# Kernel tuning notes

Measured on AMD Instinct MI355X. Metric: run time of the kernel, lower is better.

## Reference

```python
import jax, jax.numpy as jnp
import numpy as np

B, T, DNA_DIM = 8, 8192, 4
HID, C, K = 256, 5, 16
NEG = -1e30


def setup_inputs() -> dict:
    key = jax.random.key(0)
    ks = jax.random.split(key, 9)
    sequence = jax.random.normal(ks[0], (B, T, DNA_DIM), dtype=jnp.float32)
    lengths = jax.random.randint(ks[1], (B,), T // 2, T + 1).astype(jnp.int32)
    W_enc = jax.random.normal(ks[2], (DNA_DIM, HID), dtype=jnp.float32) * 0.1
    b_enc = jnp.zeros((HID,), dtype=jnp.float32)
    W_proj = jax.random.normal(ks[3], (HID, C), dtype=jnp.float32) * 0.05
    b_proj = jnp.zeros((C,), dtype=jnp.float32)
    trans = jax.random.normal(ks[4], (C, C), dtype=jnp.float32) * 0.1
    start = jax.random.normal(ks[5], (C,), dtype=jnp.float32) * 0.1
    dur = jax.random.normal(ks[6], (C, K), dtype=jnp.float32) * 0.1  # learned duration scores
    return {"sequence": sequence, "lengths": lengths, "W_enc": W_enc, "b_enc": b_enc,
            "W_proj": W_proj, "b_proj": b_proj, "trans": trans, "start": start, "dur": dur}


def reference(sequence, lengths, W_enc, b_enc, W_proj, b_proj, trans, start, dur):
    """Encoder + semi-Markov CRF head forward.

    Returns (partition, cum_scores):
      partition  : (B,) log partition function over all segmentations up to `lengths`.
      cum_scores : (B, T+1, C) cumulative per-class emission scores (segment score
                   for span (s, t] with label c is cum[t, c] - cum[s, c]).
    """
    # --- encoder: pointwise linear + GELU ---
    hidden = jax.nn.gelu(sequence @ W_enc + b_enc)          # (B, T, HID)
    emit = hidden @ W_proj + b_proj                          # (B, T, C)

    # --- cumulative segment scores ---
    cum = jnp.concatenate(
        [jnp.zeros((B, 1, C), emit.dtype), jnp.cumsum(emit, axis=1)], axis=1
    )                                                        # (B, T+1, C)

    # prevs[:, t-1, d-1, :] = cum[:, t-d, :]   (zero-padded for t-d < 0; masked by H)
    cum_pad = jnp.pad(cum, ((0, 0), (K, 0), (0, 0)))         # (B, T+1+K, C)
    prevs = jnp.stack(
        [cum_pad[:, K - d + 1: K - d + 1 + T, :] for d in range(1, K + 1)], axis=2
    )                                                        # (B, T, K, C)
    cur = cum[:, 1:, :]                                      # (B, T, C)

    dur_t = dur.T                                            # (K, C)

    # --- semi-Markov forward DP via scan; carry = last K transition-folded alphas ---
    # H[:, d-1, :] = m[t-d] where m[j, c] = logsumexp_{c'} alpha[j, c'] + trans[c', c]
    # and m[0] = start scores.
    H0 = jnp.full((B, K, C), NEG, dtype=emit.dtype).at[:, 0, :].set(start[None, :])

    def step(H, xs):
        cur_t, prev_t = xs                                   # (B, C), (B, K, C)
        seg = cur_t[:, None, :] - prev_t                     # segment emission scores
        score = H + seg + dur_t[None, :, :]                  # (B, K, C)
        alpha = jax.nn.logsumexp(score, axis=1)              # (B, C)
        m = jax.nn.logsumexp(alpha[:, :, None] + trans[None, :, :], axis=1)  # (B, C)
        Hn = jnp.concatenate([m[:, None, :], H[:, :-1, :]], axis=1)
        return Hn, alpha

    xs = (jnp.swapaxes(cur, 0, 1), jnp.swapaxes(prevs, 0, 1))
    _, alphas = jax.lax.scan(step, H0, xs)                   # (T, B, C)

    alpha_L = alphas[lengths - 1, jnp.arange(B)]             # (B, C) at each sequence end
    partition = jax.nn.logsumexp(alpha_L, axis=-1)           # (B,)
    return partition, cum
```

## Files before the change

### kernel.cpp

```cpp
#include <hip/hip_runtime.h>
#include <hip/hip_bf16.h>

#define B_ 8
#define T_ 8192
#define HID_ 256
#define C_ 5
#define K_ 16
#define NC_ 32
#define NTILE 32
#define GSPAN 272
#define GW 276
#define GIOFF (5 * GW)
#define NFW 15

__device__ __forceinline__ float gelu_tanh(float x) {
    float u = 0.7978845608028654f * (x + 0.044715f * x * x * x);
    float e = __expf(2.0f * u);
    float th = 1.0f - 2.0f / (e + 1.0f);
    return 0.5f * x * (1.0f + th);
}

__device__ __forceinline__ float bf16lo(unsigned int u) {
    return __uint_as_float(u << 16);
}
__device__ __forceinline__ float bf16hi(unsigned int u) {
    return __uint_as_float(u & 0xffff0000u);
}
template <int CTRL>
__device__ __forceinline__ float dppf(float x) {
    return __uint_as_float((unsigned int)__builtin_amdgcn_mov_dpp(
        (int)__float_as_uint(x), CTRL, 0xF, 0xF, true));
}

__global__ __launch_bounds__(256) void encoder_kernel(
    const float* __restrict__ seq, const float* __restrict__ W_enc,
    const float* __restrict__ b_enc, const float* __restrict__ W_proj,
    const float* __restrict__ b_proj, float* __restrict__ emitA,
    float* __restrict__ emitB, float* __restrict__ PA)
{
    __shared__ float4 we[128];
    __shared__ float  be[128];
    __shared__ float  wp[128 * C_];
    __shared__ float  prd[4][C_];
    int tid = threadIdx.x;
    int half = blockIdx.x >> 8;
    int blk  = blockIdx.x & 255;
    int h0 = half * 128;
    if (tid < 128) {
        int h = h0 + tid;
        we[tid] = make_float4(W_enc[0*HID_+h], W_enc[1*HID_+h], W_enc[2*HID_+h], W_enc[3*HID_+h]);
        be[tid] = b_enc[h];
    }
    for (int i = tid; i < 128 * C_; i += 256) wp[i] = W_proj[h0 * C_ + i];
    __syncthreads();
    int b = blk >> 5;
    int tile = blk & 31;
    int t = tile * 256 + tid;
    float4 s = reinterpret_cast<const float4*>(seq)[(size_t)b * T_ + t];
    float a0, a1, a2, a3, a4;
    if (half == 0) { a0 = b_proj[0]; a1 = b_proj[1]; a2 = b_proj[2]; a3 = b_proj[3]; a4 = b_proj[4]; }
    else           { a0 = a1 = a2 = a3 = a4 = 0.0f; }
    #pragma unroll 8
    for (int h = 0; h < 128; ++h) {
        float4 w = we[h];
        float pre = be[h] + s.x*w.x + s.y*w.y + s.z*w.z + s.w*w.w;
        float hd = gelu_tanh(pre);
        a0 = fmaf(hd, wp[h*C_+0], a0);
        a1 = fmaf(hd, wp[h*C_+1], a1);
        a2 = fmaf(hd, wp[h*C_+2], a2);
        a3 = fmaf(hd, wp[h*C_+3], a3);
        a4 = fmaf(hd, wp[h*C_+4], a4);
    }
    float* em = half ? emitB : emitA;
    size_t base = (size_t)b * C_ * T_ + t;
    em[base + 0*T_] = a0;
    em[base + 1*T_] = a1;
    em[base + 2*T_] = a2;
    em[base + 3*T_] = a3;
    em[base + 4*T_] = a4;
    float s0 = a0, s1 = a1, s2 = a2, s3 = a3, s4 = a4;
    #pragma unroll
    for (int off = 1; off < 64; off <<= 1) {
        s0 += __shfl_xor(s0, off, 64);
        s1 += __shfl_xor(s1, off, 64);
        s2 += __shfl_xor(s2, off, 64);
        s3 += __shfl_xor(s3, off, 64);
        s4 += __shfl_xor(s4, off, 64);
    }
    int lane = tid & 63, wv = tid >> 6;
    if (lane == 0) { prd[wv][0]=s0; prd[wv][1]=s1; prd[wv][2]=s2; prd[wv][3]=s3; prd[wv][4]=s4; }
    __syncthreads();
    if (tid < C_) {
        float t4 = (prd[0][tid] + prd[1][tid]) + (prd[2][tid] + prd[3][tid]);
        PA[((half * B_ + b) * NTILE + tile) * C_ + tid] = t4;
    }
}

__global__ __launch_bounds__(64) void cumwrite_kernel(
    const float* __restrict__ emitA, const float* __restrict__ emitB,
    const float* __restrict__ PA, float* __restrict__ cum)
{
    int bx = blockIdx.x;
    int tile = bx & (NTILE - 1);
    int bc = bx >> 5;
    int b = bc / C_, c = bc - b * C_;
    int lane = threadIdx.x;
    float v = 0.0f;
    if (lane < NTILE && lane < tile)
        v = PA[((0 * B_ + b) * NTILE + lane) * C_ + c]
          + PA[((1 * B_ + b) * NTILE + lane) * C_ + c];
    #pragma unroll
    for (int o = 32; o; o >>= 1) v += __shfl_xor(v, o, 64);
    const float* eA = emitA + ((size_t)b * C_ + c) * T_;
    const float* eB = emitB + ((size_t)b * C_ + c) * T_;
    float* cb = cum + (size_t)b * (T_ + 1) * C_;
    if (tile == 0 && lane == 0) cb[c] = 0.0f;
    float carry = v;
    #pragma unroll
    for (int i = 0; i < 4; ++i) {
        int idx = tile * 256 + i * 64 + lane;
        float e = eA[idx] + eB[idx];
        float si = e;
        #pragma unroll
        for (int o = 1; o < 64; o <<= 1) {
            float n = __shfl_up(si, o, 64);
            if (lane >= o) si += n;
        }
        cb[(size_t)(idx + 1) * C_ + c] = carry + si;
        carry += __shfl(si, 63, 64);
    }
}

#define DOT16(PP, OUT)                                                        \
    {                                                                         \
        float q0, q1, q2, q3;                                                 \
        q0 = W[0] * ed[(0 + (PP)) & 15];                                      \
        q1 = W[1] * ed[(1 + (PP)) & 15];                                      \
        q2 = W[2] * ed[(2 + (PP)) & 15];                                      \
        q3 = W[3] * ed[(3 + (PP)) & 15];                                      \
        q0 = fmaf(W[4],  ed[(4  + (PP)) & 15], q0);                           \
        q1 = fmaf(W[5],  ed[(5  + (PP)) & 15], q1);                           \
        q2 = fmaf(W[6],  ed[(6  + (PP)) & 15], q2);                           \
        q3 = fmaf(W[7],  ed[(7  + (PP)) & 15], q3);                           \
        q0 = fmaf(W[8],  ed[(8  + (PP)) & 15], q0);                           \
        q1 = fmaf(W[9],  ed[(9  + (PP)) & 15], q1);                           \
        q2 = fmaf(W[10], ed[(10 + (PP)) & 15], q2);                           \
        q3 = fmaf(W[11], ed[(11 + (PP)) & 15], q3);                           \
        q0 = fmaf(W[12], ed[(12 + (PP)) & 15], q0);                           \
        q1 = fmaf(W[13], ed[(13 + (PP)) & 15], q1);                           \
        q2 = fmaf(W[14], ed[(14 + (PP)) & 15], q2);                           \
        q3 = fmaf(W[15], ed[(15 + (PP)) & 15], q3);                           \
        OUT = (q0 + q1) + (q2 + q3);                                          \
    }

#define CSTEP(PP, GV, GIV, CAP)                                               \
    {                                                                         \
        P *= (GV); iP *= (GIV);                                               \
        float dtv;                                                            \
        DOT16(PP, dtv);                                                       \
        acur = P * dtv;                                                       \
        float r3  = dppf<0x113>(acur);                         \
        float r6  = dppf<0x116>(acur);                         \
        float r9  = dppf<0x119>(acur);                         \
        float r12 = dppf<0x11C>(acur);                         \
        float l3  = dppf<0x103>(acur);                         \
        float l6  = dppf<0x106>(acur);                         \
        float l9  = dppf<0x109>(acur);                         \
        float l12 = dppf<0x10C>(acur);                         \
        if (CAP) {                                                            \
            A0v = fmaf(a0w0, acur, fmaf(a0w1, r3, fmaf(a0w2, r6,              \
                  fmaf(a0w3, r9, a0w4 * r12))));                              \
        }                                                                     \
        float Sn = fmaf(wSelf, acur,                                          \
                   fmaf(wL1, r3,  fmaf(wL2, r6,  fmaf(wL3, r9,                \
                   fmaf(wL4, r12, fmaf(wR1, l3,  fmaf(wR2, l6,                \
                   fmaf(wR3, l9,  wR4 * l12))))))));                          \
        W[15 - (PP)] = Sn * iP;                                               \
    }

#define CRENORM()                                                             \
    {                                                                         \
        bool ok = (A0v > 1e-30f);                                             \
        float rr = ok ? __builtin_amdgcn_rcpf(A0v) : 1.0f;                    \
        float lz = ok ? __logf(A0v) : 0.0f;                                   \
        float f = P * rr;                                                     \
        _Pragma("unroll") for (int q = 0; q < 16; ++q) W[q] *= f;             \
        P = 1.0f; iP = 1.0f; z += lz;                                         \
    }

#define QBLK(Q)                                                               \
    {                                                                         \
        float4 vg  = *reinterpret_cast<const float4*>(gpg + tl0 + (Q));       \
        float4 vgi = *reinterpret_cast<const float4*>(gpi + tl0 + (Q));       \
        CSTEP((Q)+0, vg.x, vgi.x, 0); CSTEP((Q)+1, vg.y, vgi.y, 0);           \
        CSTEP((Q)+2, vg.z, vgi.z, 0);                                         \
        CSTEP((Q)+3, vg.w, vgi.w, ((Q) == 4 || (Q) == 12));                   \
    }

#define TS(PP, GV, GIV)                                                       \
    if ((PP) < rem) {                                                         \
        CSTEP(PP, GV, GIV, ((PP) == 7 || (PP) == 15));                        \
        if ((PP) == rem - 1) Afin = acur;                                     \
        if ((((PP) & 7) == 7) && ((PP) < rem - 1)) CRENORM();                 \
    }

#define TQ(Q)                                                                 \
    if ((Q) < rem) {                                                          \
        float4 vg  = *reinterpret_cast<const float4*>(gpg + tl0 + (Q));       \
        float4 vgi = *reinterpret_cast<const float4*>(gpi + tl0 + (Q));       \
        TS((Q)+0, vg.x, vgi.x); TS((Q)+1, vg.y, vgi.y);                       \
        TS((Q)+2, vg.z, vgi.z); TS((Q)+3, vg.w, vgi.w);                       \
    }

__global__ __launch_bounds__(448) void chunk_kernel(
    const float* __restrict__ emitA, const float* __restrict__ emitB,
    const int* __restrict__ lengths, const float* __restrict__ trans,
    const float* __restrict__ dur, __hip_bfloat16* __restrict__ Mout,
    float* __restrict__ Rout, float* __restrict__ ezOut,
    float* __restrict__ Zmx)
{
    __shared__ float gg[2 * 5 * GW];
    __shared__ float zsh[80];
    __shared__ float zred;
    int blk = blockIdx.x;
    int b = blk >> 5, k = blk & (NC_ - 1);
    int len = lengths[b];
    int s = (k * len) >> 5;
    int e = ((k + 1) * len) >> 5;
    int L = e - s;
    int tid = threadIdx.x;

    for (int i = tid; i < C_ * GSPAN; i += 448) {
        int cc = i / GSPAN, j = i - cc * GSPAN;
        int pos = s - 16 + j;
        float g = 1.0f, gi = 1.0f;
        if (pos >= 0 && j < 16 + L) {
            size_t gx = ((size_t)b * C_ + cc) * T_ + pos;
            float ev = emitA[gx] + emitB[gx];
            g = __expf(ev); gi = __expf(-ev);
        }
        gg[cc * GW + j] = g;
        gg[GIOFF + cc * GW + j] = gi;
    }
    __syncthreads();

    int lane = tid & 63, wv = tid >> 6;
    int row16 = lane >> 4;
    int sub = lane & 15;
    int c = sub / 3; if (c > 4) c = 4;
    int colIdx = sub - c * 3;
    int col = wv * 12 + row16 * 3 + colIdx;
    bool active = (sub < 15) && (col < 80);

    const float* gpg = &gg[c * GW + 16];
    const float* gpi = &gg[GIOFF + c * GW + 16];

    float ed[K_];
    #pragma unroll
    for (int j = 0; j < K_; ++j) ed[j] = __expf(dur[c * K_ + j]);

    float gate = active ? 1.0f : 0.0f;
    float eTf[C_];
    #pragma unroll
    for (int x = 0; x < C_; ++x) eTf[x] = __expf(trans[x * C_ + c]) * gate;
    float wSelf = eTf[c];
    float wL1 = (c >= 1) ? eTf[c-1] : 0.0f;
    float wL2 = (c >= 2) ? eTf[c-2] : 0.0f;
    float wL3 = (c >= 3) ? eTf[c-3] : 0.0f;
    float wL4 = (c >= 4) ? eTf[c-4] : 0.0f;
    float wR1 = (c + 1 <= 4) ? eTf[c+1] : 0.0f;
    float wR2 = (c + 2 <= 4) ? eTf[c+2] : 0.0f;
    float wR3 = (c + 3 <= 4) ? eTf[c+3] : 0.0f;
    float wR4 = (c + 4 <= 4) ? eTf[c+4] : 0.0f;
    float a0w0 = (c == 0) ? gate : 0.0f;
    float a0w1 = (c == 1) ? gate : 0.0f;
    float a0w2 = (c == 2) ? gate : 0.0f;
    float a0w3 = (c == 3) ? gate : 0.0f;
    float a0w4 = (c == 4) ? gate : 0.0f;

    int j0 = col / 5, c0 = col - j0 * 5;
    float sv = 1.0f;
    for (int j = 16 - j0; j < 16; ++j) sv *= gg[c0 * GW + j];
    float W[K_];
    #pragma unroll
    for (int q = 0; q < K_; ++q)
        W[q] = (active && c == c0 && q == j0) ? sv : 0.0f;

    float P = 1.0f, iP = 1.0f, z = 0.0f;
    float acur = 0.0f, Afin = 0.0f, A0v = 0.0f;

    int nfull = (L - 1) >> 4;
    int rem = L - (nfull << 4);
    int tl0 = 0;

    for (int bi = 0; bi < nfull; ++bi) {
        QBLK(0); QBLK(4);
        CRENORM();
        QBLK(8); QBLK(12);
        CRENORM();
        tl0 += 16;
    }
    TQ(0); TQ(4); TQ(8); TQ(12);

    size_t cid = (size_t)b * NC_ + k;
    int pn = L & 15;
    if (k == NC_ - 1) {
        if (active) {
            Rout[(size_t)b * 400 + (size_t)col * C_ + c] = Afin;
            if (c == 0) zsh[col] = z;
        }
    } else {
        float lm = 0.0f;
        if (active) {
            #pragma unroll
            for (int slot = 0; slot < K_; ++slot) {
                int j = (slot + pn) & 15;
                float pr = 1.0f;
                for (int i2 = 0; i2 < j; ++i2)
                    pr *= gg[GIOFF + c * GW + 16 + L - 1 - i2];
                float vv = W[slot] * P * pr;
                W[slot] = vv;
                lm = fmaxf(lm, vv);
            }
        }
        float m = lm;
        m = fmaxf(m, dppf<0x103>(lm)); m = fmaxf(m, dppf<0x106>(lm));
        m = fmaxf(m, dppf<0x109>(lm)); m = fmaxf(m, dppf<0x10C>(lm));
        m = fmaxf(m, dppf<0x113>(lm)); m = fmaxf(m, dppf<0x116>(lm));
        m = fmaxf(m, dppf<0x119>(lm)); m = fmaxf(m, dppf<0x11C>(lm));
        float cmax = m;
        float inv = (cmax > 0.0f) ? 1.0f / cmax : 0.0f;
        if (active) {
            __hip_bfloat16* mb = Mout + cid * 6400 + (size_t)col * 80;
            #pragma unroll
            for (int slot = 0; slot < K_; ++slot) {
                int j = (slot + pn) & 15;
                mb[j * C_ + c] = __float2bfloat16(W[slot] * inv);
            }
            if (c == 0) zsh[col] = (cmax > 0.0f) ? z + __logf(cmax) : -3.0e38f;
        }
    }
    __syncthreads();
    if (tid < 64) {
        float m = zsh[tid];
        if (tid < 16) m = fmaxf(m, zsh[tid + 64]);
        #pragma unroll
        for (int off = 32; off; off >>= 1) m = fmaxf(m, __shfl_xor(m, off, 64));
        if (tid == 0) zred = m;
    }
    __syncthreads();
    float zm = zred;
    if (tid == 0) Zmx[cid] = zm;
    if (active && c == 0) ezOut[cid * 80 + col] = __expf(zsh[col] - zm);
}

__global__ __launch_bounds__(320) void chain_kernel(
    const __hip_bfloat16* __restrict__ Mst, const float* __restrict__ ezZ,
    const float* __restrict__ Zmx, const float* __restrict__ Rst,
    const float* __restrict__ startv, float* __restrict__ Uvec,
    float* __restrict__ Xvec, float* __restrict__ Zu, float* __restrict__ Zx)
{
    __shared__ float Ml[2][80 * 82];
    __shared__ float vin[80], sv[80], part[4][80];
    __shared__ float red;
    int b = blockIdx.x >> 1;
    int dir = blockIdx.x & 1;
    int tid = threadIdx.x;
    float Z = 0.0f;
    int nmat = (dir == 0) ? NFW : (NC_ - 1 - NFW);

    if (dir == 0) {
        if (tid < 80) vin[tid] = (tid < C_) ? __expf(startv[tid]) : 0.0f;
        __syncthreads();
    } else {
        size_t last = (size_t)b * NC_ + NC_ - 1;
        if (tid < 80) {
            const float* R = Rst + (size_t)b * 400 + (size_t)tid * C_;
            float rs = ((R[0] + R[1]) + (R[2] + R[3])) + R[4];
            sv[tid] = rs * ezZ[last * 80 + tid];
        }
        __syncthreads();
        if (tid < 64) {
            float m = sv[tid];
            if (tid < 16) m = fmaxf(m, sv[tid + 64]);
            #pragma unroll
            for (int o = 32; o; o >>= 1) m = fmaxf(m, __shfl_xor(m, o, 64));
            if (tid == 0) red = m;
        }
        __syncthreads();
        float rm = red;
        if (tid < 80) vin[tid] = sv[tid] / rm;
        Z = Zmx[b * NC_ + NC_ - 1] + __logf(rm);
        __syncthreads();
    }

    int mk0 = (dir == 0) ? 0 : NC_ - 2;
    {
        const unsigned int* mg = (const unsigned int*)(Mst + (size_t)(b * NC_ + mk0) * 6400);
        #pragma unroll
        for (int i = 0; i < 10; ++i) {
            unsigned int u = mg[tid + 320 * i];
            int idx = (tid + 320 * i) * 2;
            int r = idx / 80, cc = idx - r * 80;
            Ml[0][r * 82 + cc]     = bf16lo(u);
            Ml[0][r * 82 + cc + 1] = bf16hi(u);
        }
    }
    __syncthreads();

    int cur = 0;
    int grp = tid / 80, r = tid - grp * 80;
    for (int it = 0; it < nmat; ++it) {
        int k  = (dir == 0) ? it : (NC_ - 2 - it);
        int kn = (dir == 0) ? k + 1 : k - 1;
        bool more = (it + 1 < nmat);
        size_t cid = (size_t)b * NC_ + k;

        unsigned int mu[10];
        if (more) {
            const unsigned int* mg = (const unsigned int*)(Mst + ((size_t)b * NC_ + kn) * 6400);
            #pragma unroll
            for (int i = 0; i < 10; ++i) mu[i] = mg[tid + 320 * i];
        }
        float ezv = 0.0f;
        if (tid < 80) {
            ezv = ezZ[cid * 80 + tid];
            sv[tid] = (dir == 0) ? vin[tid] * ezv : vin[tid];
        }
        __syncthreads();

        float p = 0.0f;
        if (dir == 0) {
            int q0 = grp * 20;
            #pragma unroll
            for (int i = 0; i < 20; ++i)
                p = fmaf(Ml[cur][(q0 + i) * 82 + r], sv[q0 + i], p);
        } else {
            int rowb = grp * 20;
            #pragma unroll
            for (int i = 0; i < 20; ++i)
                p = fmaf(Ml[cur][r * 82 + rowb + i], sv[rowb + i], p);
        }
        part[grp][r] = p;
        if (more) {
            #pragma unroll
            for (int i = 0; i < 10; ++i) {
                unsigned int u = mu[i];
                int idx = (tid + 320 * i) * 2;
                int rr = idx / 80, cc = idx - rr * 80;
                Ml[cur ^ 1][rr * 82 + cc]     = bf16lo(u);
                Ml[cur ^ 1][rr * 82 + cc + 1] = bf16hi(u);
            }
        }
        __syncthreads();

        Z += Zmx[cid];
        bool rn = ((it & 3) == 3) || (it == nmat - 1);
        if (tid < 80) {
            float nv = (part[0][tid] + part[1][tid]) + (part[2][tid] + part[3][tid]);
            if (dir == 1) nv *= ezv;
            if (rn) sv[tid] = nv; else vin[tid] = nv;
        }
        if (rn) {
            __syncthreads();
            if (tid < 64) {
                float m = sv[tid];
                if (tid < 16) m = fmaxf(m, sv[tid + 64]);
                #pragma unroll
                for (int o = 32; o; o >>= 1) m = fmaxf(m, __shfl_xor(m, o, 64));
                if (tid == 0) red = m;
            }
            __syncthreads();
            float rm = red;
            if (tid < 80) vin[tid] = sv[tid] / rm;
            Z += __logf(rm);
        }
        cur ^= 1;
    }

    if (dir == 0) {
        if (tid < 80) Xvec[b * 80 + tid] = vin[tid];
        if (tid == 0) Zx[b] = Z;
    } else {
        if (tid < 80) Uvec[b * 80 + tid] = vin[tid];
        if (tid == 0) Zu[b] = Z;
    }
}

__global__ __launch_bounds__(512) void meet_kernel(
    const float* __restrict__ Uvec, const float* __restrict__ Xvec,
    const float* __restrict__ Zu, const float* __restrict__ Zx,
    float* __restrict__ partition)
{
    int tid = threadIdx.x;
    int b = tid >> 6, lane = tid & 63;
    float v = Uvec[b * 80 + lane] * Xvec[b * 80 + lane];
    if (lane < 16) v += Uvec[b * 80 + 64 + lane] * Xvec[b * 80 + 64 + lane];
    #pragma unroll
    for (int off = 32; off; off >>= 1) v += __shfl_xor(v, off, 64);
    if (lane == 0) partition[b] = Zu[b] + Zx[b] + __logf(v);
}

extern "C" void kernel_launch(void* const* d_in, const int* in_sizes, int n_in,
                              void* d_out, int out_size, void* d_ws, size_t ws_size,
                              hipStream_t stream) {
    (void)in_sizes; (void)n_in; (void)out_size; (void)ws_size;
    const float* seq    = (const float*)d_in[0];
    const int*   lens   = (const int*)  d_in[1];
    const float* W_enc  = (const float*)d_in[2];
    const float* b_enc  = (const float*)d_in[3];
    const float* W_proj = (const float*)d_in[4];
    const float* b_proj = (const float*)d_in[5];
    const float* trans  = (const float*)d_in[6];
    const float* startv = (const float*)d_in[7];
    const float* dur    = (const float*)d_in[8];

    float* out       = (float*)d_out;
    float* partition = out;
    float* cum       = out + B_;

    float* emitA = (float*)d_ws;
    float* emitB = emitA + (size_t)B_ * C_ * T_;
    __hip_bfloat16* Mst = (__hip_bfloat16*)(emitB + (size_t)B_ * C_ * T_);
    float* Rst = (float*)(Mst + (size_t)B_ * NC_ * 6400);
    float* ezS = Rst + (size_t)B_ * 400;
    float* Zmx = ezS + (size_t)B_ * NC_ * 80;
    float* PA  = Zmx + (size_t)B_ * NC_;
    float* Uv  = PA  + 2 * B_ * NTILE * C_;
    float* Xv  = Uv  + B_ * 80;
    float* Zu  = Xv  + B_ * 80;
    float* Zx  = Zu  + B_;

    encoder_kernel<<<512, 256, 0, stream>>>(seq, W_enc, b_enc, W_proj, b_proj, emitA, emitB, PA);
    chunk_kernel<<<B_ * NC_, 448, 0, stream>>>(emitA, emitB, lens, trans, dur, Mst, Rst, ezS, Zmx);
    cumwrite_kernel<<<B_ * C_ * NTILE, 64, 0, stream>>>(emitA, emitB, PA, cum);
    chain_kernel<<<16, 320, 0, stream>>>(Mst, ezS, Zmx, Rst, startv, Uv, Xv, Zu, Zx);
    meet_kernel<<<1, 512, 0, stream>>>(Uv, Xv, Zu, Zx, partition);
}
```

Baseline: 92.45 us.

## Store chain matrices in per-thread layout and drop LDS staging in chain kernel

The producer now writes the 80x80 bf16 transfer matrices transposed for forward-direction chunks, so each chain thread owns a contiguous run of 20 elements it can load straight into registers. The chain kernel no longer unpacks matrices into a double-buffered shared array. It keeps the current matrix in registers, prefetches the next one, and reads the input vector with float4 loads. Renormalisation now runs every 8 steps instead of every 4, which cuts barriers and reductions but leaves more room for values to grow between rescales. Per-thread global loads of 10 consecutive words are less coalesced than the previous strided pattern.

After: 87.61 us. 1.06x faster.

```diff
diff --git a/kernel.cpp b/kernel.cpp
--- a/kernel.cpp
+++ b/kernel.cpp
@@ -331,11 +331,19 @@
         float cmax = m;
         float inv = (cmax > 0.0f) ? 1.0f / cmax : 0.0f;
         if (active) {
-            __hip_bfloat16* mb = Mout + cid * 6400 + (size_t)col * 80;
-            #pragma unroll
-            for (int slot = 0; slot < K_; ++slot) {
-                int j = (slot + pn) & 15;
-                mb[j * C_ + c] = __float2bfloat16(W[slot] * inv);
+            __hip_bfloat16* mb = Mout + cid * 6400;
+            if (k < NFW) {
+                #pragma unroll
+                for (int slot = 0; slot < K_; ++slot) {
+                    int j = (slot + pn) & 15;
+                    mb[(j * C_ + c) * 80 + col] = __float2bfloat16(W[slot] * inv);
+                }
+            } else {
+                #pragma unroll
+                for (int slot = 0; slot < K_; ++slot) {
+                    int j = (slot + pn) & 15;
+                    mb[(size_t)col * 80 + j * C_ + c] = __float2bfloat16(W[slot] * inv);
+                }
             }
             if (c == 0) zsh[col] = (cmax > 0.0f) ? z + __logf(cmax) : -3.0e38f;
         }
@@ -360,12 +368,16 @@
     const float* __restrict__ startv, float* __restrict__ Uvec,
     float* __restrict__ Xvec, float* __restrict__ Zu, float* __restrict__ Zx)
 {
-    __shared__ float Ml[2][80 * 82];
-    __shared__ float vin[80], sv[80], part[4][80];
+    __shared__ __align__(16) float vin[80];
+    __shared__ __align__(16) float sv[80];
+    __shared__ __align__(16) float part[4][80];
     __shared__ float red;
     int b = blockIdx.x >> 1;
     int dir = blockIdx.x & 1;
     int tid = threadIdx.x;
+    int grp = tid / 80, r = tid - grp * 80;
+    int base = grp * 20;
+    int moff = r * 40 + grp * 10;
     float Z = 0.0f;
     int nmat = (dir == 0) ? NFW : (NC_ - 1 - NFW);
 
@@ -394,68 +406,51 @@
         __syncthreads();
     }
 
-    int mk0 = (dir == 0) ? 0 : NC_ - 2;
+    int k0 = (dir == 0) ? 0 : NC_ - 2;
+    unsigned int pm[10];
     {
-        const unsigned int* mg = (const unsigned int*)(Mst + (size_t)(b * NC_ + mk0) * 6400);
+        const unsigned int* mg = (const unsigned int*)(Mst + (size_t)(b * NC_ + k0) * 6400);
         #pragma unroll
-        for (int i = 0; i < 10; ++i) {
-            unsigned int u = mg[tid + 320 * i];
-            int idx = (tid + 320 * i) * 2;
-            int r = idx / 80, cc = idx - r * 80;
-            Ml[0][r * 82 + cc]     = bf16lo(u);
-            Ml[0][r * 82 + cc + 1] = bf16hi(u);
-        }
-    }
-    __syncthreads();
-
-    int cur = 0;
-    int grp = tid / 80, r = tid - grp * 80;
+        for (int i = 0; i < 10; ++i) pm[i] = mg[moff + i];
+    }
+
     for (int it = 0; it < nmat; ++it) {
         int k  = (dir == 0) ? it : (NC_ - 2 - it);
         int kn = (dir == 0) ? k + 1 : k - 1;
         bool more = (it + 1 < nmat);
         size_t cid = (size_t)b * NC_ + k;
 
+        float ezv = 0.0f;
+        if (tid < 80) {
+            ezv = ezZ[cid * 80 + tid];
+            sv[tid] = (dir == 0) ? vin[tid] * ezv : vin[tid];
+        }
+        __syncthreads();
+
         unsigned int mu[10];
         if (more) {
             const unsigned int* mg = (const unsigned int*)(Mst + ((size_t)b * NC_ + kn) * 6400);
             #pragma unroll
-            for (int i = 0; i < 10; ++i) mu[i] = mg[tid + 320 * i];
-        }
-        float ezv = 0.0f;
-        if (tid < 80) {
-            ezv = ezZ[cid * 80 + tid];
-            sv[tid] = (dir == 0) ? vin[tid] * ezv : vin[tid];
-        }
+            for (int i = 0; i < 10; ++i) mu[i] = mg[moff + i];
+        }
+
+        float xv[20];
+        #pragma unroll
+        for (int i2 = 0; i2 < 5; ++i2)
+            *reinterpret_cast<float4*>(&xv[4 * i2]) =
+                *reinterpret_cast<const float4*>(&sv[base + 4 * i2]);
+        float p = 0.0f;
+        #pragma unroll
+        for (int i = 0; i < 10; ++i) {
+            unsigned int u = pm[i];
+            p = fmaf(bf16lo(u), xv[2 * i + 0], p);
+            p = fmaf(bf16hi(u), xv[2 * i + 1], p);
+        }
+        part[grp][r] = p;
         __syncthreads();
 
-        float p = 0.0f;
-        if (dir == 0) {
-            int q0 = grp * 20;
-            #pragma unroll
-            for (int i = 0; i < 20; ++i)
-                p = fmaf(Ml[cur][(q0 + i) * 82 + r], sv[q0 + i], p);
-        } else {
-            int rowb = grp * 20;
-            #pragma unroll
-            for (int i = 0; i < 20; ++i)
-                p = fmaf(Ml[cur][r * 82 + rowb + i], sv[rowb + i], p);
-        }
-        part[grp][r] = p;
-        if (more) {
-            #pragma unroll
-            for (int i = 0; i < 10; ++i) {
-                unsigned int u = mu[i];
-                int idx = (tid + 320 * i) * 2;
-                int rr = idx / 80, cc = idx - rr * 80;
-                Ml[cur ^ 1][rr * 82 + cc]     = bf16lo(u);
-                Ml[cur ^ 1][rr * 82 + cc + 1] = bf16hi(u);
-            }
-        }
-        __syncthreads();
-
         Z += Zmx[cid];
-        bool rn = ((it & 3) == 3) || (it == nmat - 1);
+        bool rn = ((it & 7) == 7) || (it == nmat - 1);
         if (tid < 80) {
             float nv = (part[0][tid] + part[1][tid]) + (part[2][tid] + part[3][tid]);
             if (dir == 1) nv *= ezv;
@@ -475,7 +470,8 @@
             if (tid < 80) vin[tid] = sv[tid] / rm;
             Z += __logf(rm);
         }
-        cur ^= 1;
+        #pragma unroll
+        for (int i = 0; i < 10; ++i) pm[i] = mu[i];
     }
 
     if (dir == 0) {
```
